# Kernel tuning notes

Hardware: AMD Instinct MI355X
Metric: run time of the kernel (lower is better)

The kernel has to match this reference:

```python
import jax, jax.numpy as jnp
import numpy as np

B, L, C, H = 2, 2048, 1024, 16
D = C // H  # dim per head

def setup_inputs() -> dict:
    key = jax.random.key(0)
    ks = jax.random.split(key, 13)
    s = 1.0 / np.sqrt(C)
    inp = {
        "query": jax.random.normal(ks[0], (B, L, C), jnp.float32),
        "key": jax.random.normal(ks[1], (B, L, C), jnp.float32),
        "value": jax.random.normal(ks[2], (B, L, C), jnp.float32),
        "mask": jax.random.randint(ks[3], (B, 1, L, L), 0, 2, jnp.int32),
        "WQ": jax.random.normal(ks[4], (C, C), jnp.float32) * s,
        "bQ": jnp.zeros((C,), jnp.float32),
        "WK": jax.random.normal(ks[5], (C, C), jnp.float32) * s,
        "bK": jnp.zeros((C,), jnp.float32),
        "WV": jax.random.normal(ks[6], (C, C), jnp.float32) * s,
        "bV": jnp.zeros((C,), jnp.float32),
        "WO": jax.random.normal(ks[7], (C, C), jnp.float32) * s,
        "bO": jnp.zeros((C,), jnp.float32),
    }
    return inp

def reference(query, key, value, mask, WQ, bQ, WK, bK, WV, bV, WO, bO):
    b = query.shape[0]
    # projections: x @ W + b  (W stored [in, out])
    Q = query @ WQ + bQ
    K = key @ WK + bK
    V = value @ WV + bV
    # [B, L, C] -> [B, H, L, D]
    def split_heads(x):
        return x.reshape(b, -1, H, D).transpose(0, 2, 1, 3)
    Qh, Kh, Vh = split_heads(Q), split_heads(K), split_heads(V)
    scores = jnp.einsum("bhqd,bhkd->bhqk", Qh, Kh) / jnp.sqrt(jnp.float32(D))
    scores = jnp.where(mask == 0, jnp.float32(-1e9), scores)
    attn = jax.nn.softmax(scores, axis=-1)
    Z = jnp.einsum("bhqk,bhkd->bhqd", attn, Vh)  # [B, H, L, D]
    Z = Z.transpose(0, 2, 1, 3).reshape(b, Q.shape[1], C)
    return Z @ WO + bO
```

## Files before the change

### kernel.cpp

```cpp
#include <hip/hip_runtime.h>

#define BB 2
#define LL 2048
#define CC 1024
#define HH 16
#define DD 64
#define MM (BB * LL)

typedef __bf16 bf16x8 __attribute__((ext_vector_type(8)));
typedef float  f32x4  __attribute__((ext_vector_type(4)));

__device__ __forceinline__ unsigned short f2bf(float x) {
    unsigned u = __float_as_uint(x);
    unsigned r = (u + 0x7FFFu + ((u >> 16) & 1u)) >> 16;
    return (unsigned short)r;
}
__device__ __forceinline__ float bf2f(unsigned short h) {
    return __uint_as_float(((unsigned)h) << 16);
}
__device__ __forceinline__ void split2(float x, unsigned short& hi, unsigned short& lo) {
    hi = f2bf(x);
    lo = f2bf(x - bf2f(hi));
}

#define GLOAD_LDS16(g, l)                                                      \
    __builtin_amdgcn_global_load_lds(                                          \
        (const __attribute__((address_space(1))) void*)(g),                    \
        (__attribute__((address_space(3))) void*)(l), 16, 0, 0)

#define MFMA16(a, b, c) __builtin_amdgcn_mfma_f32_16x16x32_bf16((a), (b), (c), 0, 0, 0)

__global__ __launch_bounds__(256) void w_prep(
    const float* __restrict__ W, unsigned short* __restrict__ Whi,
    unsigned short* __restrict__ Wlo)
{
    __shared__ float T[64][65];
    const int tid = threadIdx.x;
    const int k0 = blockIdx.x * 64, n0 = blockIdx.y * 64;
    #pragma unroll
    for (int p = 0; p < 4; ++p) {
        const int idx = tid + p * 256;
        const int r = idx >> 4, c4 = idx & 15;
        float4 v = *(const float4*)&W[(size_t)(k0 + r) * CC + n0 + c4 * 4];
        T[r][c4 * 4 + 0] = v.x; T[r][c4 * 4 + 1] = v.y;
        T[r][c4 * 4 + 2] = v.z; T[r][c4 * 4 + 3] = v.w;
    }
    __syncthreads();
    #pragma unroll
    for (int p = 0; p < 16; ++p) {
        const int idx = tid + p * 256;
        const int n = idx >> 6, k = idx & 63;
        unsigned short hi, lo;
        split2(T[k][n], hi, lo);
        Whi[(size_t)(n0 + n) * CC + k0 + k] = hi;
        Wlo[(size_t)(n0 + n) * CC + k0 + k] = lo;
    }
}

__global__ __launch_bounds__(256) void x_prep(
    const float* __restrict__ X, unsigned short* __restrict__ Xhi,
    unsigned short* __restrict__ Xlo)
{
    const size_t i = (size_t)blockIdx.x * 256 + threadIdx.x;
    float4 v = *(const float4*)&X[i * 4];
    unsigned short h0, l0, h1, l1, h2, l2, h3, l3;
    split2(v.x, h0, l0); split2(v.y, h1, l1);
    split2(v.z, h2, l2); split2(v.w, h3, l3);
    ushort4 hv; hv.x = h0; hv.y = h1; hv.z = h2; hv.w = h3;
    ushort4 lv; lv.x = l0; lv.y = l1; lv.z = l2; lv.w = l3;
    *(ushort4*)&Xhi[i * 4] = hv;
    *(ushort4*)&Xlo[i * 4] = lv;
}

__global__ __launch_bounds__(256) void vt_prep(
    const float* __restrict__ Vp, unsigned short* __restrict__ Vt)
{
    __shared__ float T[64][65];
    const int tid = threadIdx.x;
    const int t = blockIdx.x, h = blockIdx.y, b = blockIdx.z;
    #pragma unroll
    for (int p = 0; p < 4; ++p) {
        const int idx = tid + p * 256;
        const int r = idx >> 4, c4 = idx & 15;
        float4 v = *(const float4*)&Vp[(size_t)(b * LL + t * 64 + r) * CC + h * DD + c4 * 4];
        T[r][c4 * 4 + 0] = v.x; T[r][c4 * 4 + 1] = v.y;
        T[r][c4 * 4 + 2] = v.z; T[r][c4 * 4 + 3] = v.w;
    }
    __syncthreads();
    unsigned short* out = Vt + (size_t)(b * HH + h) * DD * LL;
    #pragma unroll
    for (int p = 0; p < 16; ++p) {
        const int idx = tid + p * 256;
        const int d = idx >> 6, l = idx & 63;
        out[(size_t)d * LL + t * 64 + l] = f2bf(T[l][d]);
    }
}

__global__ __launch_bounds__(256) void mask_pack(
    const int* __restrict__ mask, unsigned int* __restrict__ mp)
{
    const size_t wi = (size_t)blockIdx.x * 256 + threadIdx.x;
    const int* src = mask + wi * 32;
    unsigned int v = 0;
    #pragma unroll
    for (int j = 0; j < 32; j += 4) {
        int4 m4 = *(const int4*)&src[j];
        if (m4.x != 0) v |= 1u << (j + 0);
        if (m4.y != 0) v |= 1u << (j + 1);
        if (m4.z != 0) v |= 1u << (j + 2);
        if (m4.w != 0) v |= 1u << (j + 3);
    }
    mp[wi] = v;
}

template <int MODE>
__global__ __launch_bounds__(256) void gemm_split(
    const unsigned short* __restrict__ Ahi, const unsigned short* __restrict__ Alo,
    const unsigned short* __restrict__ Bhi, const unsigned short* __restrict__ Blo,
    const float* __restrict__ bias, float scale,
    float* __restrict__ Yf,
    unsigned short* __restrict__ Yhi, unsigned short* __restrict__ Ylo)
{
    __shared__ __align__(16) unsigned short Ah[128 * 32];
    __shared__ __align__(16) unsigned short Al[128 * 32];
    __shared__ __align__(16) unsigned short Bh[128 * 32];
    __shared__ __align__(16) unsigned short Bl[128 * 32];

    const int tid  = threadIdx.x;
    const int lane = tid & 63, w = tid >> 6;
    const int wr = w >> 1, wc = w & 1;
    const int lr = lane & 15, kg = lane >> 4;
    const int row0 = blockIdx.x * 128, col0 = blockIdx.y * 128;

    f32x4 acc[4][4];
    #pragma unroll
    for (int i = 0; i < 4; ++i)
        #pragma unroll
        for (int j = 0; j < 4; ++j)
            acc[i][j] = (f32x4){0.f, 0.f, 0.f, 0.f};

    const int srow = lane >> 2;
    const int sk   = (lane & 3) * 8;

    for (int kt = 0; kt < CC / 32; ++kt) {
        const int k0 = kt * 32;
        #pragma unroll
        for (int c = 0; c < 2; ++c) {
            const int chunk = w * 2 + c;
            const int r = chunk * 16 + srow;
            GLOAD_LDS16(Ahi + (size_t)(row0 + r) * CC + k0 + sk, Ah + chunk * 512);
            GLOAD_LDS16(Alo + (size_t)(row0 + r) * CC + k0 + sk, Al + chunk * 512);
            GLOAD_LDS16(Bhi + (size_t)(col0 + r) * CC + k0 + sk, Bh + chunk * 512);
            GLOAD_LDS16(Blo + (size_t)(col0 + r) * CC + k0 + sk, Bl + chunk * 512);
        }
        __syncthreads();

        bf16x8 ah[4], al[4], bh[4], bl[4];
        const int ko = kg * 8;
        #pragma unroll
        for (int i = 0; i < 4; ++i) {
            ah[i] = *(const bf16x8*)&Ah[(wr * 64 + i * 16 + lr) * 32 + ko];
            al[i] = *(const bf16x8*)&Al[(wr * 64 + i * 16 + lr) * 32 + ko];
            bh[i] = *(const bf16x8*)&Bh[(wc * 64 + i * 16 + lr) * 32 + ko];
            bl[i] = *(const bf16x8*)&Bl[(wc * 64 + i * 16 + lr) * 32 + ko];
        }
        #pragma unroll
        for (int i = 0; i < 4; ++i)
            #pragma unroll
            for (int j = 0; j < 4; ++j) {
                acc[i][j] = MFMA16(ah[i], bh[j], acc[i][j]);
                acc[i][j] = MFMA16(ah[i], bl[j], acc[i][j]);
                acc[i][j] = MFMA16(al[i], bh[j], acc[i][j]);
            }
        __syncthreads();
    }

    #pragma unroll
    for (int j = 0; j < 4; ++j) {
        const int n = col0 + wc * 64 + j * 16 + lr;
        const float bv = bias[n];
        #pragma unroll
        for (int i = 0; i < 4; ++i) {
            const int mbase = row0 + wr * 64 + i * 16 + kg * 4;
            #pragma unroll
            for (int r = 0; r < 4; ++r) {
                const float v = (acc[i][j][r] + bv) * scale;
                const int m = mbase + r;
                if (MODE == 0) {
                    Yf[(size_t)m * CC + n] = v;
                } else {
                    const int bb = m >> 11, ll = m & (LL - 1);
                    const int hh = n >> 6, dd = n & 63;
                    const size_t o = ((size_t)(bb * HH + hh) * LL + ll) * DD + dd;
                    unsigned short hi, lo;
                    split2(v, hi, lo);
                    Yhi[o] = hi; Ylo[o] = lo;
                }
            }
        }
    }
}

__global__ __launch_bounds__(256) void flash_mfma(
    const unsigned short* __restrict__ Qhi, const unsigned short* __restrict__ Qlo,
    const unsigned short* __restrict__ Khi, const unsigned short* __restrict__ Klo,
    const unsigned short* __restrict__ Vt,  const unsigned int* __restrict__ maskp,
    unsigned short* __restrict__ Zhi, unsigned short* __restrict__ Zlo)
{
    __shared__ __align__(16) unsigned short Kh_s[64 * 64];
    __shared__ __align__(16) unsigned short Kl_s[64 * 64];
    __shared__ __align__(16) unsigned short Vt_s[64 * 64];
    __shared__ __align__(16) unsigned short Ps[4][16 * 72];

    const int tid  = threadIdx.x;
    const int lane = tid & 63, w = tid >> 6;
    const int lr = lane & 15, kg = lane >> 4;
    const int q0 = blockIdx.x * 64;
    const int h = blockIdx.y, b = blockIdx.z;
    const size_t bh = (size_t)(b * HH + h);

    const unsigned short* Qhi_b = Qhi + bh * LL * DD;
    const unsigned short* Qlo_b = Qlo + bh * LL * DD;
    const unsigned short* Khi_b = Khi + bh * LL * DD;
    const unsigned short* Klo_b = Klo + bh * LL * DD;
    const unsigned short* Vt_b  = Vt  + bh * DD * LL;

    const int qrow = q0 + w * 16 + lr;
    bf16x8 qh[2], ql[2];
    #pragma unroll
    for (int s = 0; s < 2; ++s) {
        qh[s] = *(const bf16x8*)&Qhi_b[(size_t)qrow * DD + s * 32 + kg * 8];
        ql[s] = *(const bf16x8*)&Qlo_b[(size_t)qrow * DD + s * 32 + kg * 8];
    }

    f32x4 oacc[4];
    float m_r[4], l_r[4];
    #pragma unroll
    for (int r = 0; r < 4; ++r) {
        oacc[r] = (f32x4){0.f, 0.f, 0.f, 0.f};
        m_r[r] = -3.0e38f; l_r[r] = 0.f;
    }

    for (int kt = 0; kt < LL / 64; ++kt) {
        #pragma unroll
        for (int c = 0; c < 2; ++c) {
            const int chunk = w * 2 + c;
            const int rowi = chunk * 8 + (lane >> 3);
            const int cb   = (lane & 7) * 16;
            const int scb  = cb ^ ((rowi & 7) << 4);
            GLOAD_LDS16(Khi_b + (size_t)(kt * 64 + rowi) * DD + scb / 2, Kh_s + chunk * 512);
            GLOAD_LDS16(Klo_b + (size_t)(kt * 64 + rowi) * DD + scb / 2, Kl_s + chunk * 512);
            GLOAD_LDS16(Vt_b + (size_t)rowi * LL + kt * 64 + scb / 2,    Vt_s + chunk * 512);
        }
        __syncthreads();

        f32x4 sacc[4];
        #pragma unroll
        for (int j = 0; j < 4; ++j) sacc[j] = (f32x4){0.f, 0.f, 0.f, 0.f};
        #pragma unroll
        for (int j = 0; j < 4; ++j) {
            const int krow = j * 16 + lr;
            const int rswz = (krow & 7) << 4;
            #pragma unroll
            for (int s = 0; s < 2; ++s) {
                const int cb = (s * 64 + kg * 16) ^ rswz;
                bf16x8 kh = *(const bf16x8*)((const char*)Kh_s + krow * 128 + cb);
                bf16x8 kl = *(const bf16x8*)((const char*)Kl_s + krow * 128 + cb);
                sacc[j] = MFMA16(qh[s], kh, sacc[j]);
                sacc[j] = MFMA16(qh[s], kl, sacc[j]);
                sacc[j] = MFMA16(ql[s], kh, sacc[j]);
            }
        }

        #pragma unroll
        for (int r = 0; r < 4; ++r) {
            const int qr = q0 + w * 16 + kg * 4 + r;
            const unsigned int* mb = maskp + ((size_t)b * LL + qr) * (LL / 32) + kt * 2;
            const unsigned int m0 = mb[0], m1 = mb[1];
            float p[4];
            float mx = -3.0e38f;
            #pragma unroll
            for (int j = 0; j < 4; ++j) {
                const unsigned int wsel = (j < 2) ? m0 : m1;
                const int bit = (j & 1) * 16 + lr;
                if (((wsel >> bit) & 1u) == 0u) sacc[j][r] = -1.0e9f;
                mx = fmaxf(mx, sacc[j][r]);
            }
            #pragma unroll
            for (int off = 1; off < 16; off <<= 1)
                mx = fmaxf(mx, __shfl_xor(mx, off, 16));
            const float mnew = fmaxf(m_r[r], mx);
            const float f = __expf(m_r[r] - mnew);
            m_r[r] = mnew;
            float sum = 0.f;
            #pragma unroll
            for (int j = 0; j < 4; ++j) {
                p[j] = __expf(sacc[j][r] - mnew);
                sum += p[j];
            }
            #pragma unroll
            for (int off = 1; off < 16; off <<= 1)
                sum += __shfl_xor(sum, off, 16);
            l_r[r] = l_r[r] * f + sum;
            #pragma unroll
            for (int jd = 0; jd < 4; ++jd) oacc[jd][r] *= f;
            #pragma unroll
            for (int j = 0; j < 4; ++j)
                Ps[w][(kg * 4 + r) * 72 + j * 16 + lr] = f2bf(p[j]);
        }
        __syncthreads();

        #pragma unroll
        for (int s = 0; s < 2; ++s) {
            bf16x8 pa = *(const bf16x8*)&Ps[w][lr * 72 + s * 32 + kg * 8];
            #pragma unroll
            for (int jd = 0; jd < 4; ++jd) {
                const int vrow = jd * 16 + lr;
                const int cb = (s * 64 + kg * 16) ^ ((vrow & 7) << 4);
                bf16x8 vb = *(const bf16x8*)((const char*)Vt_s + vrow * 128 + cb);
                oacc[jd] = MFMA16(pa, vb, oacc[jd]);
            }
        }
        __syncthreads();
    }

    #pragma unroll
    for (int r = 0; r < 4; ++r) {
        const float inv = 1.0f / l_r[r];
        const int qg = q0 + w * 16 + kg * 4 + r;
        const size_t rowb = ((size_t)(b * LL + qg)) * CC + h * DD;
        #pragma unroll
        for (int jd = 0; jd < 4; ++jd) {
            unsigned short hi, lo;
            split2(oacc[jd][r] * inv, hi, lo);
            Zhi[rowb + jd * 16 + lr] = hi;
            Zlo[rowb + jd * 16 + lr] = lo;
        }
    }
}

extern "C" void kernel_launch(void* const* d_in, const int* in_sizes, int n_in,
                              void* d_out, int out_size, void* d_ws, size_t ws_size,
                              hipStream_t stream)
{
    const float* query = (const float*)d_in[0];
    const float* key   = (const float*)d_in[1];
    const float* value = (const float*)d_in[2];
    const int*   mask  = (const int*)d_in[3];
    const float* WQ = (const float*)d_in[4];
    const float* bQ = (const float*)d_in[5];
    const float* WK = (const float*)d_in[6];
    const float* bK = (const float*)d_in[7];
    const float* WV = (const float*)d_in[8];
    const float* bV = (const float*)d_in[9];
    const float* WO = (const float*)d_in[10];
    const float* bO = (const float*)d_in[11];
    float* out = (float*)d_out;

    char* ws = (char*)d_ws;
    const size_t MB = 1024 * 1024;
    unsigned short* WQt_hi = (unsigned short*)(ws + 0 * MB);
    unsigned short* WQt_lo = (unsigned short*)(ws + 2 * MB);
    unsigned short* WKt_hi = (unsigned short*)(ws + 4 * MB);
    unsigned short* WKt_lo = (unsigned short*)(ws + 6 * MB);
    unsigned short* WVt_hi = (unsigned short*)(ws + 8 * MB);
    unsigned short* WVt_lo = (unsigned short*)(ws + 10 * MB);
    unsigned short* WOt_hi = (unsigned short*)(ws + 12 * MB);
    unsigned short* WOt_lo = (unsigned short*)(ws + 14 * MB);
    unsigned short* Xhi    = (unsigned short*)(ws + 16 * MB);
    unsigned short* Xlo    = (unsigned short*)(ws + 24 * MB);
    unsigned short* Qh_hi  = (unsigned short*)(ws + 32 * MB);
    unsigned short* Qh_lo  = (unsigned short*)(ws + 40 * MB);
    unsigned short* Kh_hi  = (unsigned short*)(ws + 48 * MB);
    unsigned short* Kh_lo  = (unsigned short*)(ws + 56 * MB);
    float*          Vp     = (float*)(ws + 64 * MB);
    unsigned short* Vt     = (unsigned short*)(ws + 80 * MB);
    unsigned int*   maskp  = (unsigned int*)(ws + 88 * MB);

    const dim3 blk(256);
    const dim3 wgrid(CC / 64, CC / 64);
    w_prep<<<wgrid, blk, 0, stream>>>(WQ, WQt_hi, WQt_lo);
    w_prep<<<wgrid, blk, 0, stream>>>(WK, WKt_hi, WKt_lo);
    w_prep<<<wgrid, blk, 0, stream>>>(WV, WVt_hi, WVt_lo);
    w_prep<<<wgrid, blk, 0, stream>>>(WO, WOt_hi, WOt_lo);
    mask_pack<<<dim3((BB * LL * (LL / 32)) / 256), blk, 0, stream>>>(mask, maskp);

    const dim3 ggrid(MM / 128, CC / 128);
    const dim3 xgrid((size_t)MM * CC / 4 / 256);

    x_prep<<<xgrid, blk, 0, stream>>>(query, Xhi, Xlo);
    gemm_split<1><<<ggrid, blk, 0, stream>>>(Xhi, Xlo, WQt_hi, WQt_lo, bQ, 0.125f,
                                             nullptr, Qh_hi, Qh_lo);
    x_prep<<<xgrid, blk, 0, stream>>>(key, Xhi, Xlo);
    gemm_split<1><<<ggrid, blk, 0, stream>>>(Xhi, Xlo, WKt_hi, WKt_lo, bK, 1.0f,
                                             nullptr, Kh_hi, Kh_lo);
    x_prep<<<xgrid, blk, 0, stream>>>(value, Xhi, Xlo);
    gemm_split<0><<<ggrid, blk, 0, stream>>>(Xhi, Xlo, WVt_hi, WVt_lo, bV, 1.0f,
                                             Vp, nullptr, nullptr);
    vt_prep<<<dim3(LL / 64, HH, BB), blk, 0, stream>>>(Vp, Vt);

    flash_mfma<<<dim3(LL / 64, HH, BB), blk, 0, stream>>>(
        Qh_hi, Qh_lo, Kh_hi, Kh_lo, Vt, maskp, Xhi, Xlo);

    gemm_split<0><<<ggrid, blk, 0, stream>>>(Xhi, Xlo, WOt_hi, WOt_lo, bO, 1.0f,
                                             out, nullptr, nullptr);
}
```

Before: 493.9 us.

## Double-buffer GEMM and flash LDS tiles, use exp2 softmax with lazy rescaling

Both the split-bf16 GEMM and the flash attention kernel now keep two LDS buffers and issue the next tile's global-to-LDS loads before computing on the current one, which hides load latency and drops one barrier per iteration. The GEMM LDS tile gets an XOR swizzle to cut bank conflicts. Softmax moves to exp2, with log2(e) folded into the Q projection scale, and the running max and accumulators are only rescaled when some row's max grows by more than 8. MFMA sections are wrapped in s_setprio, and the bf16 conversions use native casts. The cost is twice the LDS per block, which may lower occupancy, and P values up to 2^8 before normalisation, which slightly changes numerics.

```diff
diff --git a/kernel.cpp b/kernel.cpp
--- a/kernel.cpp
+++ b/kernel.cpp
@@ -10,17 +10,24 @@
 typedef __bf16 bf16x8 __attribute__((ext_vector_type(8)));
 typedef float  f32x4  __attribute__((ext_vector_type(4)));
 
+#define LOG2E 1.44269504088896340736f
+#if defined(__has_builtin)
+#if __has_builtin(__builtin_amdgcn_exp2f)
+#define EXP2F(x) __builtin_amdgcn_exp2f(x)
+#else
+#define EXP2F(x) exp2f(x)
+#endif
+#else
+#define EXP2F(x) exp2f(x)
+#endif
+
 __device__ __forceinline__ unsigned short f2bf(float x) {
-    unsigned u = __float_as_uint(x);
-    unsigned r = (u + 0x7FFFu + ((u >> 16) & 1u)) >> 16;
-    return (unsigned short)r;
-}
-__device__ __forceinline__ float bf2f(unsigned short h) {
-    return __uint_as_float(((unsigned)h) << 16);
+    return __builtin_bit_cast(unsigned short, (__bf16)x);
 }
 __device__ __forceinline__ void split2(float x, unsigned short& hi, unsigned short& lo) {
-    hi = f2bf(x);
-    lo = f2bf(x - bf2f(hi));
+    __bf16 h = (__bf16)x;
+    hi = __builtin_bit_cast(unsigned short, h);
+    lo = __builtin_bit_cast(unsigned short, (__bf16)(x - (float)h));
 }
 
 #define GLOAD_LDS16(g, l)                                                      \
@@ -121,10 +128,10 @@
     float* __restrict__ Yf,
     unsigned short* __restrict__ Yhi, unsigned short* __restrict__ Ylo)
 {
-    __shared__ __align__(16) unsigned short Ah[128 * 32];
-    __shared__ __align__(16) unsigned short Al[128 * 32];
-    __shared__ __align__(16) unsigned short Bh[128 * 32];
-    __shared__ __align__(16) unsigned short Bl[128 * 32];
+    __shared__ __align__(16) unsigned short Ah[2][128 * 32];
+    __shared__ __align__(16) unsigned short Al[2][128 * 32];
+    __shared__ __align__(16) unsigned short Bh[2][128 * 32];
+    __shared__ __align__(16) unsigned short Bl[2][128 * 32];
 
     const int tid  = threadIdx.x;
     const int lane = tid & 63, w = tid >> 6;
@@ -140,29 +147,38 @@
             acc[i][j] = (f32x4){0.f, 0.f, 0.f, 0.f};
 
     const int srow = lane >> 2;
-    const int sk   = (lane & 3) * 8;
-
-    for (int kt = 0; kt < CC / 32; ++kt) {
-        const int k0 = kt * 32;
-        #pragma unroll
-        for (int c = 0; c < 2; ++c) {
-            const int chunk = w * 2 + c;
-            const int r = chunk * 16 + srow;
-            GLOAD_LDS16(Ahi + (size_t)(row0 + r) * CC + k0 + sk, Ah + chunk * 512);
-            GLOAD_LDS16(Alo + (size_t)(row0 + r) * CC + k0 + sk, Al + chunk * 512);
-            GLOAD_LDS16(Bhi + (size_t)(col0 + r) * CC + k0 + sk, Bh + chunk * 512);
-            GLOAD_LDS16(Blo + (size_t)(col0 + r) * CC + k0 + sk, Bl + chunk * 512);
-        }
-        __syncthreads();
+    const int ssl  = ((lane & 3) ^ ((srow >> 1) & 3)) * 8;
+
+    #define GSTAGE(bufi, kt_)                                                  \
+        {                                                                      \
+            const int k0_ = (kt_) * 32;                                        \
+            _Pragma("unroll")                                                  \
+            for (int c = 0; c < 2; ++c) {                                      \
+                const int chunk = w * 2 + c;                                   \
+                const int r = chunk * 16 + srow;                               \
+                GLOAD_LDS16(Ahi + (size_t)(row0 + r) * CC + k0_ + ssl, &Ah[bufi][chunk * 512]); \
+                GLOAD_LDS16(Alo + (size_t)(row0 + r) * CC + k0_ + ssl, &Al[bufi][chunk * 512]); \
+                GLOAD_LDS16(Bhi + (size_t)(col0 + r) * CC + k0_ + ssl, &Bh[bufi][chunk * 512]); \
+                GLOAD_LDS16(Blo + (size_t)(col0 + r) * CC + k0_ + ssl, &Bl[bufi][chunk * 512]); \
+            }                                                                  \
+        }
+
+    GSTAGE(0, 0);
+    __syncthreads();
+
+    const int NT = CC / 32;
+    for (int kt = 0; kt < NT; ++kt) {
+        const int cur = kt & 1;
+        if (kt + 1 < NT) GSTAGE(cur ^ 1, kt + 1);
 
         bf16x8 ah[4], al[4], bh[4], bl[4];
-        const int ko = kg * 8;
+        const int ko = (kg ^ ((lr >> 1) & 3)) * 8;
         #pragma unroll
         for (int i = 0; i < 4; ++i) {
-            ah[i] = *(const bf16x8*)&Ah[(wr * 64 + i * 16 + lr) * 32 + ko];
-            al[i] = *(const bf16x8*)&Al[(wr * 64 + i * 16 + lr) * 32 + ko];
-            bh[i] = *(const bf16x8*)&Bh[(wc * 64 + i * 16 + lr) * 32 + ko];
-            bl[i] = *(const bf16x8*)&Bl[(wc * 64 + i * 16 + lr) * 32 + ko];
+            ah[i] = *(const bf16x8*)&Ah[cur][(wr * 64 + i * 16 + lr) * 32 + ko];
+            al[i] = *(const bf16x8*)&Al[cur][(wr * 64 + i * 16 + lr) * 32 + ko];
+            bh[i] = *(const bf16x8*)&Bh[cur][(wc * 64 + i * 16 + lr) * 32 + ko];
+            bl[i] = *(const bf16x8*)&Bl[cur][(wc * 64 + i * 16 + lr) * 32 + ko];
         }
         #pragma unroll
         for (int i = 0; i < 4; ++i)
@@ -174,6 +190,7 @@
             }
         __syncthreads();
     }
+    #undef GSTAGE
 
     #pragma unroll
     for (int j = 0; j < 4; ++j) {
@@ -207,10 +224,10 @@
     const unsigned short* __restrict__ Vt,  const unsigned int* __restrict__ maskp,
     unsigned short* __restrict__ Zhi, unsigned short* __restrict__ Zlo)
 {
-    __shared__ __align__(16) unsigned short Kh_s[64 * 64];
-    __shared__ __align__(16) unsigned short Kl_s[64 * 64];
-    __shared__ __align__(16) unsigned short Vt_s[64 * 64];
-    __shared__ __align__(16) unsigned short Ps[4][16 * 72];
+    __shared__ __align__(16) unsigned short Kh_s[2][64 * 64];
+    __shared__ __align__(16) unsigned short Kl_s[2][64 * 64];
+    __shared__ __align__(16) unsigned short Vt_s[2][64 * 64];
+    __shared__ __align__(16) __bf16 Ps[4][16 * 72];
 
     const int tid  = threadIdx.x;
     const int lane = tid & 63, w = tid >> 6;
@@ -241,22 +258,32 @@
         m_r[r] = -3.0e38f; l_r[r] = 0.f;
     }
 
-    for (int kt = 0; kt < LL / 64; ++kt) {
-        #pragma unroll
-        for (int c = 0; c < 2; ++c) {
-            const int chunk = w * 2 + c;
-            const int rowi = chunk * 8 + (lane >> 3);
-            const int cb   = (lane & 7) * 16;
-            const int scb  = cb ^ ((rowi & 7) << 4);
-            GLOAD_LDS16(Khi_b + (size_t)(kt * 64 + rowi) * DD + scb / 2, Kh_s + chunk * 512);
-            GLOAD_LDS16(Klo_b + (size_t)(kt * 64 + rowi) * DD + scb / 2, Kl_s + chunk * 512);
-            GLOAD_LDS16(Vt_b + (size_t)rowi * LL + kt * 64 + scb / 2,    Vt_s + chunk * 512);
-        }
-        __syncthreads();
+    #define FSTAGE(bufi, kt_)                                                  \
+        {                                                                      \
+            _Pragma("unroll")                                                  \
+            for (int c = 0; c < 2; ++c) {                                      \
+                const int chunk = w * 2 + c;                                   \
+                const int rowi = chunk * 8 + (lane >> 3);                      \
+                const int cb   = (lane & 7) * 16;                              \
+                const int scb  = cb ^ ((rowi & 7) << 4);                       \
+                GLOAD_LDS16(Khi_b + (size_t)((kt_) * 64 + rowi) * DD + scb / 2, &Kh_s[bufi][chunk * 512]); \
+                GLOAD_LDS16(Klo_b + (size_t)((kt_) * 64 + rowi) * DD + scb / 2, &Kl_s[bufi][chunk * 512]); \
+                GLOAD_LDS16(Vt_b + (size_t)rowi * LL + (kt_) * 64 + scb / 2,    &Vt_s[bufi][chunk * 512]); \
+            }                                                                  \
+        }
+
+    FSTAGE(0, 0);
+    __syncthreads();
+
+    const int NT = LL / 64;
+    for (int kt = 0; kt < NT; ++kt) {
+        const int cur = kt & 1;
+        if (kt + 1 < NT) FSTAGE(cur ^ 1, kt + 1);
 
         f32x4 sacc[4];
         #pragma unroll
         for (int j = 0; j < 4; ++j) sacc[j] = (f32x4){0.f, 0.f, 0.f, 0.f};
+        __builtin_amdgcn_s_setprio(1);
         #pragma unroll
         for (int j = 0; j < 4; ++j) {
             const int krow = j * 16 + lr;
@@ -264,20 +291,21 @@
             #pragma unroll
             for (int s = 0; s < 2; ++s) {
                 const int cb = (s * 64 + kg * 16) ^ rswz;
-                bf16x8 kh = *(const bf16x8*)((const char*)Kh_s + krow * 128 + cb);
-                bf16x8 kl = *(const bf16x8*)((const char*)Kl_s + krow * 128 + cb);
+                bf16x8 kh = *(const bf16x8*)((const char*)&Kh_s[cur][0] + krow * 128 + cb);
+                bf16x8 kl = *(const bf16x8*)((const char*)&Kl_s[cur][0] + krow * 128 + cb);
                 sacc[j] = MFMA16(qh[s], kh, sacc[j]);
                 sacc[j] = MFMA16(qh[s], kl, sacc[j]);
                 sacc[j] = MFMA16(ql[s], kh, sacc[j]);
             }
         }
-
+        __builtin_amdgcn_s_setprio(0);
+
+        float mxr[4];
         #pragma unroll
         for (int r = 0; r < 4; ++r) {
             const int qr = q0 + w * 16 + kg * 4 + r;
             const unsigned int* mb = maskp + ((size_t)b * LL + qr) * (LL / 32) + kt * 2;
             const unsigned int m0 = mb[0], m1 = mb[1];
-            float p[4];
             float mx = -3.0e38f;
             #pragma unroll
             for (int j = 0; j < 4; ++j) {
@@ -289,27 +317,39 @@
             #pragma unroll
             for (int off = 1; off < 16; off <<= 1)
                 mx = fmaxf(mx, __shfl_xor(mx, off, 16));
-            const float mnew = fmaxf(m_r[r], mx);
-            const float f = __expf(m_r[r] - mnew);
-            m_r[r] = mnew;
+            mxr[r] = mx;
+        }
+
+        const float g = fmaxf(fmaxf(mxr[0] - m_r[0], mxr[1] - m_r[1]),
+                              fmaxf(mxr[2] - m_r[2], mxr[3] - m_r[3]));
+        if (!__all(g <= 8.0f)) {
+            #pragma unroll
+            for (int r = 0; r < 4; ++r) {
+                const float mnew = fmaxf(m_r[r], mxr[r]);
+                const float f = EXP2F(m_r[r] - mnew);
+                m_r[r] = mnew;
+                l_r[r] *= f;
+                #pragma unroll
+                for (int jd = 0; jd < 4; ++jd) oacc[jd][r] *= f;
+            }
+        }
+
+        #pragma unroll
+        for (int r = 0; r < 4; ++r) {
             float sum = 0.f;
             #pragma unroll
             for (int j = 0; j < 4; ++j) {
-                p[j] = __expf(sacc[j][r] - mnew);
-                sum += p[j];
+                const float p = EXP2F(sacc[j][r] - m_r[r]);
+                sum += p;
+                Ps[w][(kg * 4 + r) * 72 + j * 16 + lr] = (__bf16)p;
             }
             #pragma unroll
             for (int off = 1; off < 16; off <<= 1)
                 sum += __shfl_xor(sum, off, 16);
-            l_r[r] = l_r[r] * f + sum;
-            #pragma unroll
-            for (int jd = 0; jd < 4; ++jd) oacc[jd][r] *= f;
-            #pragma unroll
-            for (int j = 0; j < 4; ++j)
-                Ps[w][(kg * 4 + r) * 72 + j * 16 + lr] = f2bf(p[j]);
-        }
-        __syncthreads();
-
+            l_r[r] += sum;
+        }
+
+        __builtin_amdgcn_s_setprio(1);
         #pragma unroll
         for (int s = 0; s < 2; ++s) {
             bf16x8 pa = *(const bf16x8*)&Ps[w][lr * 72 + s * 32 + kg * 8];
@@ -317,12 +357,14 @@
             for (int jd = 0; jd < 4; ++jd) {
                 const int vrow = jd * 16 + lr;
                 const int cb = (s * 64 + kg * 16) ^ ((vrow & 7) << 4);
-                bf16x8 vb = *(const bf16x8*)((const char*)Vt_s + vrow * 128 + cb);
+                bf16x8 vb = *(const bf16x8*)((const char*)&Vt_s[cur][0] + vrow * 128 + cb);
                 oacc[jd] = MFMA16(pa, vb, oacc[jd]);
             }
         }
+        __builtin_amdgcn_s_setprio(0);
         __syncthreads();
     }
+    #undef FSTAGE
 
     #pragma unroll
     for (int r = 0; r < 4; ++r) {
@@ -389,8 +431,8 @@
     const dim3 xgrid((size_t)MM * CC / 4 / 256);
 
     x_prep<<<xgrid, blk, 0, stream>>>(query, Xhi, Xlo);
-    gemm_split<1><<<ggrid, blk, 0, stream>>>(Xhi, Xlo, WQt_hi, WQt_lo, bQ, 0.125f,
-                                             nullptr, Qh_hi, Qh_lo);
+    gemm_split<1><<<ggrid, blk, 0, stream>>>(Xhi, Xlo, WQt_hi, WQt_lo, bQ,
+                                             0.125f * LOG2E, nullptr, Qh_hi, Qh_lo);
     x_prep<<<xgrid, blk, 0, stream>>>(key, Xhi, Xlo);
     gemm_split<1><<<ggrid, blk, 0, stream>>>(Xhi, Xlo, WKt_hi, WKt_lo, bK, 1.0f,
                                              nullptr, Kh_hi, Kh_lo);
```

After: 523.4 us. 1.06x slower.
